# Kernel tuning notes

Hardware: AMD Instinct MI355X
Metric: run time of the kernel (lower is better)

The kernel has to match this reference:

```python
import jax, jax.numpy as jnp
import numpy as np

N, E, G, D, L = 20000, 320000, 256, 256, 5
EPS = 1e-5


def _bn(h, g, b):
    # BatchNorm1d in training mode: biased batch statistics over the row dim
    m = h.mean(axis=0)
    v = jnp.mean((h - m) ** 2, axis=0)
    return g * (h - m) / jnp.sqrt(v + EPS) + b


def setup_inputs() -> dict:
    key = jax.random.key(0)
    ks = iter(jax.random.split(key, 40))

    def rn(shape, s=0.1):
        return jax.random.normal(next(ks), shape, dtype=jnp.float32) * s

    inp = {}
    inp['x_feats'] = jax.random.randint(next(ks), (N, 6), 0, 4)
    inp['edge_index'] = jax.random.randint(next(ks), (2, E), 0, N)
    inp['edge_attr'] = jax.random.randint(next(ks), (E, 5), 0, 2)
    inp['batch'] = jnp.sort(jax.random.randint(next(ks), (N,), 0, G))
    inp['nt1'] = rn((119, D)); inp['nt2'] = rn((4, D)); inp['nt3'] = rn((7, D))
    inp['nt4'] = rn((8, D)); inp['nt5'] = rn((5, D)); inp['nt6'] = rn((7, D))
    inp['et1'] = rn((L, 5, D)); inp['et2'] = rn((L, 4, D)); inp['et3'] = rn((L, 2, D))
    inp['et4'] = rn((L, 2, D)); inp['et5'] = rn((L, 2, D))
    inp['w1'] = rn((L, 2 * D, D)); inp['b1'] = rn((L, 2 * D))
    inp['w2'] = rn((L, D, 2 * D)); inp['b2'] = rn((L, D))
    inp['bng'] = 1.0 + rn((L, D)); inp['bnb'] = rn((L, D))
    inp['pw'] = rn((3, D, D)); inp['pg'] = 1.0 + rn((3, D)); inp['pb'] = rn((3, D))
    inp['ow1'] = rn((D // 2, D)); inp['ob1'] = rn((D // 2,))
    inp['ow2'] = rn((2, D // 2)); inp['ob2'] = rn((2,))
    return inp


def reference(x_feats, edge_index, edge_attr, batch,
              nt1, nt2, nt3, nt4, nt5, nt6,
              et1, et2, et3, et4, et5,
              w1, b1, w2, b2, bng, bnb,
              pw, pg, pb, ow1, ob1, ow2, ob2):
    n = x_feats.shape[0]
    # atom embedding: sum of 6 feature embeddings -> [N, D]
    h = (nt1[x_feats[:, 0]] + nt2[x_feats[:, 1]] + nt3[x_feats[:, 2]]
         + nt4[x_feats[:, 3]] + nt5[x_feats[:, 4]] + nt6[x_feats[:, 5]])
    src, dst = edge_index[0], edge_index[1]
    for l in range(L):
        # edge embedding for real edges: [E, D]
        e = (et1[l][edge_attr[:, 0]] + et2[l][edge_attr[:, 1]] + et3[l][edge_attr[:, 2]]
             + et4[l][edge_attr[:, 3]] + et5[l][edge_attr[:, 4]])
        # self-loop edges carry attr [4,0,0,0,0]
        self_e = et1[l][4] + et2[l][0] + et3[l][0] + et4[l][0] + et5[l][0]
        # message = x_j + e, scatter-add into destinations; self loops add h + self_e
        aggr = jax.ops.segment_sum(h[src] + e, dst, num_segments=n) + h + self_e
        # GIN MLP update: D -> 2D -> D
        hh = jax.nn.relu(aggr @ w1[l].T + b1[l]) @ w2[l].T + b2[l]
        # batchnorm then relu (dropout=0; the layer==num_layer branch is unreachable)
        h = jax.nn.relu(_bn(hh, bng[l], bnb[l]))
    # global mean pool over graphs
    counts = jax.ops.segment_sum(jnp.ones((n, 1), h.dtype), batch, num_segments=G)
    hg = jax.ops.segment_sum(h, batch, num_segments=G) / jnp.maximum(counts, 1.0)
    # proj head: (Linear no-bias, BN, ReLU) x2, then Linear no-bias + BN
    for i in range(3):
        hg = _bn(hg @ pw[i].T, pg[i], pb[i])
        if i < 2:
            hg = jax.nn.relu(hg)
    # output MLP: Linear -> Softplus -> Linear
    return jax.nn.softplus(hg @ ow1.T + ob1) @ ow2.T + ob2
```

## Files before the change

### kernel.cpp

```cpp
#include <hip/hip_runtime.h>

#define DD 256
#define TWO_D 512
#define NLAYER 5
#define NGRAPH 256
#define BNEPS 1e-5f

typedef __attribute__((ext_vector_type(8))) _Float16 half8;
typedef __attribute__((ext_vector_type(4))) _Float16 half4;
typedef __attribute__((ext_vector_type(4))) float f32x4;
typedef __attribute__((address_space(1))) void gvoid_t;
typedef __attribute__((address_space(3))) void svoid_t;

__global__ __launch_bounds__(256) void embed_kernel(
    const int* __restrict__ xf,
    const float* __restrict__ nt1, const float* __restrict__ nt2,
    const float* __restrict__ nt3, const float* __restrict__ nt4,
    const float* __restrict__ nt5, const float* __restrict__ nt6,
    _Float16* __restrict__ h16, int* __restrict__ deg, int N)
{
  int i = blockIdx.x;
  int j = threadIdx.x;
  if (i >= N) return;
  if (j == 0) deg[i] = 0;
  int x0 = xf[i*6+0], x1 = xf[i*6+1], x2 = xf[i*6+2];
  int x3 = xf[i*6+3], x4 = xf[i*6+4], x5 = xf[i*6+5];
  float v = nt1[x0*DD+j] + nt2[x1*DD+j] + nt3[x2*DD+j]
          + nt4[x3*DD+j] + nt5[x4*DD+j] + nt6[x5*DD+j];
  h16[(size_t)i*DD + j] = (_Float16)v;
}

__global__ __launch_bounds__(256) void hist_pack_kernel(
    const int* __restrict__ ei, const int* __restrict__ ea,
    int* __restrict__ deg, int* __restrict__ packed, int E)
{
  int e = blockIdx.x*256 + threadIdx.x;
  if (e >= E) return;
  int src = ei[e];
  int dst = ei[E + e];
  int code = (ea[e*5+0]&1) | ((ea[e*5+1]&1)<<1) | ((ea[e*5+2]&1)<<2)
           | ((ea[e*5+3]&1)<<3) | ((ea[e*5+4]&1)<<4);
  packed[e] = src | (code << 16);
  atomicAdd(&deg[dst], 1);
}

__global__ __launch_bounds__(1024) void scan_kernel(
    const int* __restrict__ deg, int* __restrict__ row_start,
    int* __restrict__ cursor, int N)
{
  __shared__ int sh[1024];
  __shared__ int carry_s;
  int t = threadIdx.x;
  if (t == 0) carry_s = 0;
  __syncthreads();
  for (int base = 0; base < N; base += 1024) {
    int carry = carry_s;
    int idx = base + t;
    int v = (idx < N) ? deg[idx] : 0;
    sh[t] = v;
    __syncthreads();
    for (int off = 1; off < 1024; off <<= 1) {
      int x = (t >= off) ? sh[t - off] : 0;
      __syncthreads();
      sh[t] += x;
      __syncthreads();
    }
    int incl = sh[t];
    if (idx < N) { int ex = carry + incl - v; row_start[idx] = ex; cursor[idx] = ex; }
    __syncthreads();
    if (t == 1023) carry_s = carry + sh[1023];
    __syncthreads();
  }
  if (t == 0) row_start[N] = carry_s;
}

__global__ __launch_bounds__(256) void scatter_kernel(
    const int* __restrict__ ei, const int* __restrict__ packed,
    int* __restrict__ cursor, int* __restrict__ esort, int E)
{
  int e = blockIdx.x*256 + threadIdx.x;
  if (e >= E) return;
  int dst = ei[E + e];
  int pos = atomicAdd(&cursor[dst], 1);
  esort[pos] = packed[e];
}

__global__ __launch_bounds__(256) void wconv_kernel(
    const float* __restrict__ w1, const float* __restrict__ w2,
    _Float16* __restrict__ w1h, _Float16* __restrict__ w2h, int n)
{
  for (int i = blockIdx.x*256 + threadIdx.x; i < n; i += gridDim.x*256) {
    w1h[i] = (_Float16)w1[i];
    w2h[i] = (_Float16)w2[i];
  }
}

__global__ __launch_bounds__(256) void etab_kernel(
    const float* __restrict__ et1, const float* __restrict__ et2,
    const float* __restrict__ et3, const float* __restrict__ et4,
    const float* __restrict__ et5, _Float16* __restrict__ etab)
{
  int b = blockIdx.x;
  int l = b / 33, c = b % 33;
  int j = threadIdx.x;
  int a0 = (c==32)?4:(c&1);
  int a1 = (c==32)?0:((c>>1)&1);
  int a2 = (c==32)?0:((c>>2)&1);
  int a3 = (c==32)?0:((c>>3)&1);
  int a4 = (c==32)?0:((c>>4)&1);
  etab[((size_t)l*33 + c)*DD + j] = (_Float16)(
      et1[(l*5+a0)*DD+j] + et2[(l*4+a1)*DD+j] + et3[(l*2+a2)*DD+j]
    + et4[(l*2+a3)*DD+j] + et5[(l*2+a4)*DD+j]);
}

__global__ __launch_bounds__(256) void bn_prep_kernel(
    float* __restrict__ stats, const float* __restrict__ g, const float* __restrict__ b,
    float* __restrict__ scsh, float inv_n)
{
  int j = threadIdx.x;
  float m = stats[j] * inv_n;
  float var = fmaxf(stats[DD + j] * inv_n - m*m, 0.f);
  float sc = g[j] * rsqrtf(var + BNEPS);
  scsh[j] = sc;
  scsh[DD + j] = b[j] - m*sc;
  stats[j] = 0.f; stats[DD + j] = 0.f;
}

template<int APPLY_BN>
__global__ __launch_bounds__(256) void aggr_kernel(
    const _Float16* __restrict__ hsrc, const _Float16* __restrict__ etab_l,
    const int* __restrict__ row_start, const int* __restrict__ esort,
    const float* __restrict__ scsh,
    _Float16* __restrict__ aggrh, int N)
{
  __shared__ __attribute__((aligned(16))) _Float16 se[33*DD];
  for (int i = threadIdx.x; i < 33*DD/8; i += 256)
    ((int4*)se)[i] = ((const int4*)etab_l)[i];
  __syncthreads();
  const int wave = threadIdx.x >> 6, lane = threadIdx.x & 63;
  const int c4 = lane << 2;
  float sc0 = 1.f, sc1 = 1.f, sc2 = 1.f, sc3 = 1.f;
  float sh0 = 0.f, sh1 = 0.f, sh2 = 0.f, sh3 = 0.f;
  if (APPLY_BN) {
    sc0 = scsh[c4+0]; sc1 = scsh[c4+1]; sc2 = scsh[c4+2]; sc3 = scsh[c4+3];
    sh0 = scsh[DD+c4+0]; sh1 = scsh[DD+c4+1]; sh2 = scsh[DD+c4+2]; sh3 = scsh[DD+c4+3];
  }
  const int W0 = blockIdx.x*4 + wave, NW = gridDim.x*4;

#define BNX(h4, out0, out1, out2, out3)                                   \
  { float t0_ = (float)(h4).x, t1_ = (float)(h4).y,                       \
          t2_ = (float)(h4).z, t3_ = (float)(h4).w;                       \
    if (APPLY_BN) {                                                       \
      t0_ = fmaxf(t0_*sc0 + sh0, 0.f); t1_ = fmaxf(t1_*sc1 + sh1, 0.f);  \
      t2_ = fmaxf(t2_*sc2 + sh2, 0.f); t3_ = fmaxf(t3_*sc3 + sh3, 0.f);  \
    }                                                                     \
    out0 = t0_; out1 = t1_; out2 = t2_; out3 = t3_; }

  for (int node = W0; node < N; node += NW) {
    int p  = row_start[node];
    int pe = row_start[node+1];
    const half4 hv = *(const half4*)(hsrc + (size_t)node*DD + c4);
    const half4 sv = *(const half4*)(se + 32*DD + c4);
    float ax, ay, az, aw;
    BNX(hv, ax, ay, az, aw);
    ax += (float)sv.x; ay += (float)sv.y; az += (float)sv.z; aw += (float)sv.w;
    for (; p + 4 <= pe; p += 4) {
      int pk0 = esort[p], pk1 = esort[p+1], pk2 = esort[p+2], pk3 = esort[p+3];
      const half4 h0 = *(const half4*)(hsrc + (size_t)(pk0 & 0xffff)*DD + c4);
      const half4 h1 = *(const half4*)(hsrc + (size_t)(pk1 & 0xffff)*DD + c4);
      const half4 h2 = *(const half4*)(hsrc + (size_t)(pk2 & 0xffff)*DD + c4);
      const half4 h3 = *(const half4*)(hsrc + (size_t)(pk3 & 0xffff)*DD + c4);
      const half4 e0 = *(const half4*)(se + (pk0 >> 16)*DD + c4);
      const half4 e1 = *(const half4*)(se + (pk1 >> 16)*DD + c4);
      const half4 e2 = *(const half4*)(se + (pk2 >> 16)*DD + c4);
      const half4 e3 = *(const half4*)(se + (pk3 >> 16)*DD + c4);
      float b0x,b0y,b0z,b0w, b1x,b1y,b1z,b1w, b2x,b2y,b2z,b2w, b3x,b3y,b3z,b3w;
      BNX(h0, b0x,b0y,b0z,b0w); BNX(h1, b1x,b1y,b1z,b1w);
      BNX(h2, b2x,b2y,b2z,b2w); BNX(h3, b3x,b3y,b3z,b3w);
      ax += (b0x+(float)e0.x) + (b1x+(float)e1.x) + (b2x+(float)e2.x) + (b3x+(float)e3.x);
      ay += (b0y+(float)e0.y) + (b1y+(float)e1.y) + (b2y+(float)e2.y) + (b3y+(float)e3.y);
      az += (b0z+(float)e0.z) + (b1z+(float)e1.z) + (b2z+(float)e2.z) + (b3z+(float)e3.z);
      aw += (b0w+(float)e0.w) + (b1w+(float)e1.w) + (b2w+(float)e2.w) + (b3w+(float)e3.w);
    }
    for (; p < pe; ++p) {
      int pk = esort[p];
      const half4 hx = *(const half4*)(hsrc + (size_t)(pk & 0xffff)*DD + c4);
      const half4 ex = *(const half4*)(se + (pk >> 16)*DD + c4);
      float bx, by, bz, bw;
      BNX(hx, bx, by, bz, bw);
      ax += bx + (float)ex.x; ay += by + (float)ex.y;
      az += bz + (float)ex.z; aw += bw + (float)ex.w;
    }
    half4 o;
    o.x = (_Float16)ax; o.y = (_Float16)ay; o.z = (_Float16)az; o.w = (_Float16)aw;
    *(half4*)(aggrh + (size_t)node*DD + c4) = o;
  }
#undef BNX
}

template<int RELU, int STATS>
__global__ __launch_bounds__(256) void gemm_bt(
    const _Float16* __restrict__ A,
    const _Float16* __restrict__ B,
    const float* __restrict__ bias,
    _Float16* __restrict__ O,
    float* __restrict__ stats,
    int K, int Nw, int Nreal)
{
  __shared__ __attribute__((aligned(16))) _Float16 lA[128*32];
  __shared__ __attribute__((aligned(16))) _Float16 lB[128*32];
  const int NT = Nw >> 7;
  const int bm = blockIdx.x / NT, bn = blockIdx.x % NT;
  const int m0 = bm << 7, n0 = bn << 7;
  const int t = threadIdx.x;
  const int wave = t >> 6, lane = t & 63;
  const int wm = wave & 1, wn = wave >> 1;
  const int r15 = lane & 15, quad = lane >> 4;
  const int srow = lane >> 2, sq = (lane & 3) << 3;
  f32x4 acc[4][4] = {};
  for (int k0 = 0; k0 < K; k0 += 32) {
    __syncthreads();
#pragma unroll
    for (int i = 0; i < 2; ++i) {
      const int seg = wave*2 + i;
      const int row = seg*16 + srow;
      __builtin_amdgcn_global_load_lds((gvoid_t*)(A + (size_t)(m0+row)*K + k0 + sq),
                                       (svoid_t*)(lA + seg*512), 16, 0, 0);
      __builtin_amdgcn_global_load_lds((gvoid_t*)(B + (size_t)(n0+row)*K + k0 + sq),
                                       (svoid_t*)(lB + seg*512), 16, 0, 0);
    }
    __syncthreads();
    half8 af[4], bfr[4];
#pragma unroll
    for (int f = 0; f < 4; ++f) {
      af[f]  = *(const half8*)(lA + (((wm<<6) + (f<<4) + r15) << 5) + (quad<<3));
      bfr[f] = *(const half8*)(lB + (((wn<<6) + (f<<4) + r15) << 5) + (quad<<3));
    }
#pragma unroll
    for (int fm = 0; fm < 4; ++fm)
#pragma unroll
      for (int fn = 0; fn < 4; ++fn)
        acc[fm][fn] = __builtin_amdgcn_mfma_f32_16x16x32_f16(af[fm], bfr[fn], acc[fm][fn], 0, 0, 0);
  }
#pragma unroll
  for (int fn = 0; fn < 4; ++fn) {
    const int col = n0 + (wn<<6) + (fn<<4) + r15;
    const float bv = bias[col];
    float s1 = 0.f, s2 = 0.f;
#pragma unroll
    for (int fm = 0; fm < 4; ++fm) {
      const int rowb = m0 + (wm<<6) + (fm<<4) + (quad<<2);
#pragma unroll
      for (int r = 0; r < 4; ++r) {
        float v = acc[fm][fn][r] + bv;
        if (RELU) v = fmaxf(v, 0.f);
        O[(size_t)(rowb + r)*Nw + col] = (_Float16)v;
        if (STATS && (rowb + r < Nreal)) { s1 += v; s2 += v*v; }
      }
    }
    if (STATS) {
      s1 += __shfl_xor(s1, 16); s1 += __shfl_xor(s1, 32);
      s2 += __shfl_xor(s2, 16); s2 += __shfl_xor(s2, 32);
      if (lane < 16) { atomicAdd(&stats[col], s1); atomicAdd(&stats[DD + col], s2); }
    }
  }
}

__global__ __launch_bounds__(256) void zero_kernel(float* __restrict__ p, int n) {
  for (int i = blockIdx.x*256 + threadIdx.x; i < n; i += gridDim.x*256) p[i] = 0.f;
}

__global__ __launch_bounds__(256) void pool_kernel(
    const _Float16* __restrict__ hh16, const float* __restrict__ scsh,
    const int* __restrict__ batch,
    float* __restrict__ hgsum, int* __restrict__ hgcnt, int N)
{
  int j = threadIdx.x;
  float sc = scsh[j], sh = scsh[DD + j];
  int r0 = blockIdx.x * 64;
  int cur = -1; float acc = 0.f; int run = 0;
  for (int r = 0; r < 64; ++r) {
    int row = r0 + r;
    if (row >= N) break;
    int g = batch[row];
    if (g != cur) {
      if (cur >= 0) {
        atomicAdd(&hgsum[(size_t)cur*DD + j], acc);
        if (j == 0) atomicAdd(&hgcnt[cur], run);
      }
      cur = g; acc = 0.f; run = 0;
    }
    float v = (float)hh16[(size_t)row*DD + j];
    acc += fmaxf(v*sc + sh, 0.f);
    run++;
  }
  if (cur >= 0) {
    atomicAdd(&hgsum[(size_t)cur*DD + j], acc);
    if (j == 0) atomicAdd(&hgcnt[cur], run);
  }
}

__global__ __launch_bounds__(256) void hgfin_kernel(
    const float* __restrict__ hgsum, const int* __restrict__ hgcnt, float* __restrict__ hg)
{
  int g = blockIdx.x, j = threadIdx.x;
  float c = (float)max(hgcnt[g], 1);
  hg[(size_t)g*DD + j] = hgsum[(size_t)g*DD + j] / c;
}

__global__ __launch_bounds__(256) void proj_gemm_kernel(
    const float* __restrict__ in, const float* __restrict__ W,
    float* __restrict__ outb, float* __restrict__ pstat)
{
  __shared__ float sA[16][17];
  __shared__ float sB[16][17];
  int tx = threadIdx.x, ty = threadIdx.y;
  int r = blockIdx.y*16 + ty;
  int c = blockIdx.x*16 + tx;
  float acc = 0.f;
  for (int k0 = 0; k0 < DD; k0 += 16) {
    sA[ty][tx] = in[(size_t)r*DD + k0 + tx];
    sB[ty][tx] = W[(size_t)(blockIdx.x*16 + ty)*DD + k0 + tx];
    __syncthreads();
#pragma unroll
    for (int kk = 0; kk < 16; ++kk) acc += sA[ty][kk] * sB[tx][kk];
    __syncthreads();
  }
  outb[(size_t)r*DD + c] = acc;
  sA[ty][tx] = acc; sB[ty][tx] = acc*acc;
  __syncthreads();
  for (int o = 8; o > 0; o >>= 1) {
    if (ty < o) { sA[ty][tx] += sA[ty+o][tx]; sB[ty][tx] += sB[ty+o][tx]; }
    __syncthreads();
  }
  if (ty == 0) { atomicAdd(&pstat[c], sA[0][tx]); atomicAdd(&pstat[DD + c], sB[0][tx]); }
}

__global__ __launch_bounds__(256) void proj_bn_kernel(
    const float* __restrict__ tin, const float* __restrict__ pstat,
    const float* __restrict__ g, const float* __restrict__ b,
    float* __restrict__ outp, int do_relu)
{
  int c = threadIdx.x, r = blockIdx.x;
  float m = pstat[c] * (1.0f/NGRAPH);
  float var = fmaxf(pstat[DD + c] * (1.0f/NGRAPH) - m*m, 0.f);
  float sc = g[c] * rsqrtf(var + BNEPS);
  float sh = b[c] - m*sc;
  float v = tin[(size_t)r*DD + c]*sc + sh;
  outp[(size_t)r*DD + c] = do_relu ? fmaxf(v, 0.f) : v;
}

__global__ __launch_bounds__(128) void out_kernel(
    const float* __restrict__ hgf, const float* __restrict__ ow1,
    const float* __restrict__ ob1, const float* __restrict__ ow2,
    const float* __restrict__ ob2, float* __restrict__ outp)
{
  __shared__ float rowv[DD];
  __shared__ float z[128];
  int r = blockIdx.x, t = threadIdx.x;
  rowv[t] = hgf[(size_t)r*DD + t];
  rowv[t + 128] = hgf[(size_t)r*DD + t + 128];
  __syncthreads();
  float a = ob1[t];
  for (int k = 0; k < DD; ++k) a += rowv[k] * ow1[(size_t)t*DD + k];
  z[t] = fmaxf(a, 0.f) + log1pf(expf(-fabsf(a)));
  __syncthreads();
  if (t < 2) {
    float o = ob2[t];
    for (int k = 0; k < 128; ++k) o += z[k] * ow2[t*128 + k];
    outp[r*2 + t] = o;
  }
}

extern "C" void kernel_launch(void* const* d_in, const int* in_sizes, int n_in,
                              void* d_out, int out_size, void* d_ws, size_t ws_size,
                              hipStream_t stream)
{
  const int* x_feats = (const int*)d_in[0];
  const int* ei      = (const int*)d_in[1];
  const int* ea      = (const int*)d_in[2];
  const int* batch   = (const int*)d_in[3];
  const float* nt1 = (const float*)d_in[4];
  const float* nt2 = (const float*)d_in[5];
  const float* nt3 = (const float*)d_in[6];
  const float* nt4 = (const float*)d_in[7];
  const float* nt5 = (const float*)d_in[8];
  const float* nt6 = (const float*)d_in[9];
  const float* et1 = (const float*)d_in[10];
  const float* et2 = (const float*)d_in[11];
  const float* et3 = (const float*)d_in[12];
  const float* et4 = (const float*)d_in[13];
  const float* et5 = (const float*)d_in[14];
  const float* w1  = (const float*)d_in[15];
  const float* b1  = (const float*)d_in[16];
  const float* w2  = (const float*)d_in[17];
  const float* b2  = (const float*)d_in[18];
  const float* bng = (const float*)d_in[19];
  const float* bnb = (const float*)d_in[20];
  const float* pw  = (const float*)d_in[21];
  const float* pg  = (const float*)d_in[22];
  const float* pb  = (const float*)d_in[23];
  const float* ow1 = (const float*)d_in[24];
  const float* ob1 = (const float*)d_in[25];
  const float* ow2 = (const float*)d_in[26];
  const float* ob2 = (const float*)d_in[27];

  const int N = in_sizes[0] / 6;
  const int E = in_sizes[1] / 2;
  const int Mp = ((N + 127) >> 7) << 7;

  unsigned char* wp = (unsigned char*)d_ws;
  size_t off = 0;
  auto carve = [&](size_t bytes) -> void* {
    void* p = wp + off;
    off += (bytes + 255) & ~(size_t)255;
    return p;
  };

  _Float16* h16      = (_Float16*)carve((size_t)N * DD * 2);
  _Float16* aggrh    = (_Float16*)carve((size_t)Mp * DD * 2);
  _Float16* hh16     = (_Float16*)carve((size_t)Mp * DD * 2);
  _Float16* hidh     = (_Float16*)carve((size_t)Mp * TWO_D * 2);
  _Float16* w1h      = (_Float16*)carve((size_t)NLAYER * TWO_D * DD * 2);
  _Float16* w2h      = (_Float16*)carve((size_t)NLAYER * TWO_D * DD * 2);
  _Float16* etabg    = (_Float16*)carve((size_t)NLAYER * 33 * DD * 2);
  float* scsh        = (float*)carve(2 * DD * 4);
  int* deg           = (int*)carve((size_t)N * 4);
  int* row_start     = (int*)carve((size_t)(N + 1) * 4);
  int* cursor        = (int*)carve((size_t)N * 4);
  int* packed        = (int*)carve((size_t)E * 4);
  int* esort         = (int*)carve((size_t)E * 4);
  float* stats       = (float*)carve(2 * DD * 4);
  float* hgsum       = (float*)carve((size_t)NGRAPH * DD * 4);
  int* hgcnt         = (int*)carve((size_t)NGRAPH * 4);
  float* pstats      = (float*)carve(3 * 2 * DD * 4);
  float* hgA         = (float*)carve((size_t)NGRAPH * DD * 4);
  float* hgB         = (float*)carve((size_t)NGRAPH * DD * 4);
  float* t0          = (float*)carve((size_t)NGRAPH * DD * 4);
  (void)ws_size; (void)n_in; (void)out_size;

  const int EB = (E + 255) / 256;
  const float inv_n = 1.0f / (float)N;

  embed_kernel<<<N, 256, 0, stream>>>(x_feats, nt1, nt2, nt3, nt4, nt5, nt6, h16, deg, N);
  hist_pack_kernel<<<EB, 256, 0, stream>>>(ei, ea, deg, packed, E);
  scan_kernel<<<1, 1024, 0, stream>>>(deg, row_start, cursor, N);
  scatter_kernel<<<EB, 256, 0, stream>>>(ei, packed, cursor, esort, E);
  wconv_kernel<<<1024, 256, 0, stream>>>(w1, w2, w1h, w2h, NLAYER * TWO_D * DD);
  etab_kernel<<<NLAYER * 33, 256, 0, stream>>>(et1, et2, et3, et4, et5, etabg);
  zero_kernel<<<128, 256, 0, stream>>>(stats, 2*DD + NGRAPH*DD + NGRAPH + 3*2*DD);

  const int gm = Mp >> 7;
  for (int l = 0; l < NLAYER; ++l) {
    if (l == 0) {
      aggr_kernel<0><<<2048, 256, 0, stream>>>(h16, etabg, row_start, esort,
                                               nullptr, aggrh, N);
    } else {
      bn_prep_kernel<<<1, 256, 0, stream>>>(stats, bng + (l-1)*DD, bnb + (l-1)*DD,
                                            scsh, inv_n);
      aggr_kernel<1><<<2048, 256, 0, stream>>>(hh16, etabg + (size_t)l*33*DD,
                                               row_start, esort, scsh, aggrh, N);
    }
    gemm_bt<1,0><<<gm * (TWO_D >> 7), 256, 0, stream>>>(
        aggrh, w1h + (size_t)l*TWO_D*DD, b1 + l*TWO_D, hidh, nullptr,
        DD, TWO_D, N);
    gemm_bt<0,1><<<gm * (DD >> 7), 256, 0, stream>>>(
        hidh, w2h + (size_t)l*DD*TWO_D, b2 + l*DD, hh16, stats,
        TWO_D, DD, N);
  }
  bn_prep_kernel<<<1, 256, 0, stream>>>(stats, bng + (NLAYER-1)*DD, bnb + (NLAYER-1)*DD,
                                        scsh, inv_n);
  pool_kernel<<<(N + 63) / 64, 256, 0, stream>>>(hh16, scsh, batch, hgsum, hgcnt, N);
  hgfin_kernel<<<NGRAPH, 256, 0, stream>>>(hgsum, hgcnt, hgA);

  dim3 pgrid(16, 16), pblk(16, 16);
  proj_gemm_kernel<<<pgrid, pblk, 0, stream>>>(hgA, pw + 0*DD*DD, t0, pstats + 0*2*DD);
  proj_bn_kernel<<<NGRAPH, 256, 0, stream>>>(t0, pstats + 0*2*DD, pg + 0*DD, pb + 0*DD, hgB, 1);
  proj_gemm_kernel<<<pgrid, pblk, 0, stream>>>(hgB, pw + 1*DD*DD, t0, pstats + 1*2*DD);
  proj_bn_kernel<<<NGRAPH, 256, 0, stream>>>(t0, pstats + 1*2*DD, pg + 1*DD, pb + 1*DD, hgA, 1);
  proj_gemm_kernel<<<pgrid, pblk, 0, stream>>>(hgA, pw + 2*DD*DD, t0, pstats + 2*2*DD);
  proj_bn_kernel<<<NGRAPH, 256, 0, stream>>>(t0, pstats + 2*2*DD, pg + 2*DD, pb + 2*DD, hgB, 0);

  out_kernel<<<NGRAPH, 128, 0, stream>>>(hgB, ow1, ob1, ow2, ob2, (float*)d_out);
}
```

Before: 597.0 us.

## Merge setup kernels, fold BN prep into consumers, stage GEMM epilogue through LDS

Merges embedding, weight conversion, edge-table build, zeroing and edge packing into one prep kernel, and splits the degree histogram into its own kernel. BatchNorm scale/shift is now computed inside the aggregation, pooling, projection and output kernels, with per-layer stats buffers. This removes the bn_prep, hgfin and proj_bn launches. The scan now does a chunked serial scan per thread instead of looping over blocks, and the GEMM epilogue stages results in LDS so global stores are 16-byte coalesced, at the cost of extra syncs.

```diff
diff --git a/kernel.cpp b/kernel.cpp
--- a/kernel.cpp
+++ b/kernel.cpp
@@ -12,36 +12,79 @@
 typedef __attribute__((address_space(1))) void gvoid_t;
 typedef __attribute__((address_space(3))) void svoid_t;
 
-__global__ __launch_bounds__(256) void embed_kernel(
+__global__ __launch_bounds__(256) void prep_kernel(
     const int* __restrict__ xf,
     const float* __restrict__ nt1, const float* __restrict__ nt2,
     const float* __restrict__ nt3, const float* __restrict__ nt4,
     const float* __restrict__ nt5, const float* __restrict__ nt6,
-    _Float16* __restrict__ h16, int* __restrict__ deg, int N)
-{
-  int i = blockIdx.x;
-  int j = threadIdx.x;
-  if (i >= N) return;
-  if (j == 0) deg[i] = 0;
-  int x0 = xf[i*6+0], x1 = xf[i*6+1], x2 = xf[i*6+2];
-  int x3 = xf[i*6+3], x4 = xf[i*6+4], x5 = xf[i*6+5];
-  float v = nt1[x0*DD+j] + nt2[x1*DD+j] + nt3[x2*DD+j]
-          + nt4[x3*DD+j] + nt5[x4*DD+j] + nt6[x5*DD+j];
-  h16[(size_t)i*DD + j] = (_Float16)v;
-}
-
-__global__ __launch_bounds__(256) void hist_pack_kernel(
+    _Float16* __restrict__ h16,
+    const float* __restrict__ w1, const float* __restrict__ w2,
+    _Float16* __restrict__ w1h, _Float16* __restrict__ w2h,
+    const float* __restrict__ et1, const float* __restrict__ et2,
+    const float* __restrict__ et3, const float* __restrict__ et4,
+    const float* __restrict__ et5, _Float16* __restrict__ etab,
+    int* __restrict__ deg, int* __restrict__ zr, int zr_words,
     const int* __restrict__ ei, const int* __restrict__ ea,
-    int* __restrict__ deg, int* __restrict__ packed, int E)
+    int* __restrict__ packed,
+    int N, int E)
+{
+  const int t = threadIdx.x;
+  const int b = blockIdx.x;
+  const int B_EMB = N;
+  const int B_WC  = 128;
+  const int B_ET  = NLAYER * 33;
+  const int B_ZR  = 96;
+
+  if (b < B_EMB) {
+    int i = b, j = t;
+    int x0 = xf[i*6+0], x1 = xf[i*6+1], x2 = xf[i*6+2];
+    int x3 = xf[i*6+3], x4 = xf[i*6+4], x5 = xf[i*6+5];
+    float v = nt1[x0*DD+j] + nt2[x1*DD+j] + nt3[x2*DD+j]
+            + nt4[x3*DD+j] + nt5[x4*DD+j] + nt6[x5*DD+j];
+    h16[(size_t)i*DD + j] = (_Float16)v;
+  } else if (b < B_EMB + B_WC) {
+    int bid = b - B_EMB;
+    int n = NLAYER * TWO_D * DD;
+    for (int i = bid*256 + t; i < n; i += B_WC*256) {
+      w1h[i] = (_Float16)w1[i];
+      w2h[i] = (_Float16)w2[i];
+    }
+  } else if (b < B_EMB + B_WC + B_ET) {
+    int bid = b - B_EMB - B_WC;
+    int l = bid / 33, c = bid % 33;
+    int j = t;
+    int a0 = (c==32)?4:(c&1);
+    int a1 = (c==32)?0:((c>>1)&1);
+    int a2 = (c==32)?0:((c>>2)&1);
+    int a3 = (c==32)?0:((c>>3)&1);
+    int a4 = (c==32)?0:((c>>4)&1);
+    etab[((size_t)l*33 + c)*DD + j] = (_Float16)(
+        et1[(l*5+a0)*DD+j] + et2[(l*4+a1)*DD+j] + et3[(l*2+a2)*DD+j]
+      + et4[(l*2+a3)*DD+j] + et5[(l*2+a4)*DD+j]);
+  } else if (b < B_EMB + B_WC + B_ET + B_ZR) {
+    int bid = b - B_EMB - B_WC - B_ET;
+    int tw = N + zr_words;
+    for (int i = bid*256 + t; i < tw; i += B_ZR*256) {
+      if (i < N) deg[i] = 0;
+      else zr[i - N] = 0;
+    }
+  } else {
+    int bid = b - B_EMB - B_WC - B_ET - B_ZR;
+    int e = bid*256 + t;
+    if (e < E) {
+      int src = ei[e];
+      int code = (ea[e*5+0]&1) | ((ea[e*5+1]&1)<<1) | ((ea[e*5+2]&1)<<2)
+               | ((ea[e*5+3]&1)<<3) | ((ea[e*5+4]&1)<<4);
+      packed[e] = src | (code << 16);
+    }
+  }
+}
+
+__global__ __launch_bounds__(256) void hist_kernel(
+    const int* __restrict__ ei, int* __restrict__ deg, int E)
 {
   int e = blockIdx.x*256 + threadIdx.x;
-  if (e >= E) return;
-  int src = ei[e];
-  int dst = ei[E + e];
-  int code = (ea[e*5+0]&1) | ((ea[e*5+1]&1)<<1) | ((ea[e*5+2]&1)<<2)
-           | ((ea[e*5+3]&1)<<3) | ((ea[e*5+4]&1)<<4);
-  packed[e] = src | (code << 16);
-  atomicAdd(&deg[dst], 1);
+  if (e < E) atomicAdd(&deg[ei[E + e]], 1);
 }
 
 __global__ __launch_bounds__(1024) void scan_kernel(
@@ -49,29 +92,26 @@
     int* __restrict__ cursor, int N)
 {
   __shared__ int sh[1024];
-  __shared__ int carry_s;
   int t = threadIdx.x;
-  if (t == 0) carry_s = 0;
+  const int CH = (N + 1023) >> 10;
+  int base = t * CH;
+  int lim = N - base; if (lim < 0) lim = 0; if (lim > CH) lim = CH;
+  int s = 0;
+  for (int i = 0; i < lim; ++i) s += deg[base + i];
+  sh[t] = s;
   __syncthreads();
-  for (int base = 0; base < N; base += 1024) {
-    int carry = carry_s;
-    int idx = base + t;
-    int v = (idx < N) ? deg[idx] : 0;
-    sh[t] = v;
-    __syncthreads();
-    for (int off = 1; off < 1024; off <<= 1) {
-      int x = (t >= off) ? sh[t - off] : 0;
-      __syncthreads();
-      sh[t] += x;
-      __syncthreads();
-    }
-    int incl = sh[t];
-    if (idx < N) { int ex = carry + incl - v; row_start[idx] = ex; cursor[idx] = ex; }
-    __syncthreads();
-    if (t == 1023) carry_s = carry + sh[1023];
-    __syncthreads();
-  }
-  if (t == 0) row_start[N] = carry_s;
+  for (int off = 1; off < 1024; off <<= 1) {
+    int x = (t >= off) ? sh[t - off] : 0;
+    __syncthreads();
+    sh[t] += x;
+    __syncthreads();
+  }
+  int run = t ? sh[t-1] : 0;
+  for (int i = 0; i < lim; ++i) {
+    row_start[base+i] = run; cursor[base+i] = run;
+    run += deg[base+i];
+  }
+  if (t == 1023) row_start[N] = sh[1023];
 }
 
 __global__ __launch_bounds__(256) void scatter_kernel(
@@ -85,52 +125,12 @@
   esort[pos] = packed[e];
 }
 
-__global__ __launch_bounds__(256) void wconv_kernel(
-    const float* __restrict__ w1, const float* __restrict__ w2,
-    _Float16* __restrict__ w1h, _Float16* __restrict__ w2h, int n)
-{
-  for (int i = blockIdx.x*256 + threadIdx.x; i < n; i += gridDim.x*256) {
-    w1h[i] = (_Float16)w1[i];
-    w2h[i] = (_Float16)w2[i];
-  }
-}
-
-__global__ __launch_bounds__(256) void etab_kernel(
-    const float* __restrict__ et1, const float* __restrict__ et2,
-    const float* __restrict__ et3, const float* __restrict__ et4,
-    const float* __restrict__ et5, _Float16* __restrict__ etab)
-{
-  int b = blockIdx.x;
-  int l = b / 33, c = b % 33;
-  int j = threadIdx.x;
-  int a0 = (c==32)?4:(c&1);
-  int a1 = (c==32)?0:((c>>1)&1);
-  int a2 = (c==32)?0:((c>>2)&1);
-  int a3 = (c==32)?0:((c>>3)&1);
-  int a4 = (c==32)?0:((c>>4)&1);
-  etab[((size_t)l*33 + c)*DD + j] = (_Float16)(
-      et1[(l*5+a0)*DD+j] + et2[(l*4+a1)*DD+j] + et3[(l*2+a2)*DD+j]
-    + et4[(l*2+a3)*DD+j] + et5[(l*2+a4)*DD+j]);
-}
-
-__global__ __launch_bounds__(256) void bn_prep_kernel(
-    float* __restrict__ stats, const float* __restrict__ g, const float* __restrict__ b,
-    float* __restrict__ scsh, float inv_n)
-{
-  int j = threadIdx.x;
-  float m = stats[j] * inv_n;
-  float var = fmaxf(stats[DD + j] * inv_n - m*m, 0.f);
-  float sc = g[j] * rsqrtf(var + BNEPS);
-  scsh[j] = sc;
-  scsh[DD + j] = b[j] - m*sc;
-  stats[j] = 0.f; stats[DD + j] = 0.f;
-}
-
 template<int APPLY_BN>
 __global__ __launch_bounds__(256) void aggr_kernel(
     const _Float16* __restrict__ hsrc, const _Float16* __restrict__ etab_l,
     const int* __restrict__ row_start, const int* __restrict__ esort,
-    const float* __restrict__ scsh,
+    const float* __restrict__ stats_prev, const float* __restrict__ g,
+    const float* __restrict__ bb, float inv_n,
     _Float16* __restrict__ aggrh, int N)
 {
   __shared__ __attribute__((aligned(16))) _Float16 se[33*DD];
@@ -139,22 +139,24 @@
   __syncthreads();
   const int wave = threadIdx.x >> 6, lane = threadIdx.x & 63;
   const int c4 = lane << 2;
-  float sc0 = 1.f, sc1 = 1.f, sc2 = 1.f, sc3 = 1.f;
-  float sh0 = 0.f, sh1 = 0.f, sh2 = 0.f, sh3 = 0.f;
+  float sc0=1.f, sc1=1.f, sc2=1.f, sc3=1.f, sh0=0.f, sh1=0.f, sh2=0.f, sh3=0.f;
   if (APPLY_BN) {
-    sc0 = scsh[c4+0]; sc1 = scsh[c4+1]; sc2 = scsh[c4+2]; sc3 = scsh[c4+3];
-    sh0 = scsh[DD+c4+0]; sh1 = scsh[DD+c4+1]; sh2 = scsh[DD+c4+2]; sh3 = scsh[DD+c4+3];
+#define MKSC(k, SC, SH) { float m_ = stats_prev[c4+k]*inv_n;                      \
+    float v_ = fmaxf(stats_prev[DD+c4+k]*inv_n - m_*m_, 0.f);                     \
+    SC = g[c4+k]*rsqrtf(v_+BNEPS); SH = bb[c4+k] - m_*SC; }
+    MKSC(0, sc0, sh0) MKSC(1, sc1, sh1) MKSC(2, sc2, sh2) MKSC(3, sc3, sh3)
+#undef MKSC
   }
   const int W0 = blockIdx.x*4 + wave, NW = gridDim.x*4;
 
-#define BNX(h4, out0, out1, out2, out3)                                   \
+#define BNX(h4, o0, o1, o2, o3)                                           \
   { float t0_ = (float)(h4).x, t1_ = (float)(h4).y,                       \
           t2_ = (float)(h4).z, t3_ = (float)(h4).w;                       \
     if (APPLY_BN) {                                                       \
       t0_ = fmaxf(t0_*sc0 + sh0, 0.f); t1_ = fmaxf(t1_*sc1 + sh1, 0.f);  \
       t2_ = fmaxf(t2_*sc2 + sh2, 0.f); t3_ = fmaxf(t3_*sc3 + sh3, 0.f);  \
     }                                                                     \
-    out0 = t0_; out1 = t1_; out2 = t2_; out3 = t3_; }
+    o0 = t0_; o1 = t1_; o2 = t2_; o3 = t3_; }
 
   for (int node = W0; node < N; node += NW) {
     int p  = row_start[node];
@@ -207,8 +209,9 @@
     float* __restrict__ stats,
     int K, int Nw, int Nreal)
 {
-  __shared__ __attribute__((aligned(16))) _Float16 lA[128*32];
-  __shared__ __attribute__((aligned(16))) _Float16 lB[128*32];
+  __shared__ __attribute__((aligned(16))) _Float16 smem[8192];
+  _Float16* lA = smem;
+  _Float16* lB = smem + 4096;
   const int NT = Nw >> 7;
   const int bm = blockIdx.x / NT, bn = blockIdx.x % NT;
   const int m0 = bm << 7, n0 = bn << 7;
@@ -242,53 +245,68 @@
       for (int fn = 0; fn < 4; ++fn)
         acc[fm][fn] = __builtin_amdgcn_mfma_f32_16x16x32_f16(af[fm], bfr[fn], acc[fm][fn], 0, 0, 0);
   }
+  float bv[4];
+#pragma unroll
+  for (int fn = 0; fn < 4; ++fn) bv[fn] = bias[n0 + (wn<<6) + (fn<<4) + r15];
+  __syncthreads();
+  _Float16* tb = smem;
 #pragma unroll
   for (int fn = 0; fn < 4; ++fn) {
-    const int col = n0 + (wn<<6) + (fn<<4) + r15;
-    const float bv = bias[col];
     float s1 = 0.f, s2 = 0.f;
 #pragma unroll
     for (int fm = 0; fm < 4; ++fm) {
-      const int rowb = m0 + (wm<<6) + (fm<<4) + (quad<<2);
+      const int lr = (wm<<6) + (fm<<4) + (quad<<2);
 #pragma unroll
       for (int r = 0; r < 4; ++r) {
-        float v = acc[fm][fn][r] + bv;
+        float v = acc[fm][fn][r] + bv[fn];
         if (RELU) v = fmaxf(v, 0.f);
-        O[(size_t)(rowb + r)*Nw + col] = (_Float16)v;
-        if (STATS && (rowb + r < Nreal)) { s1 += v; s2 += v*v; }
+        tb[(lr + r)*40 + (wn<<4) + r15] = (_Float16)v;
+        if (STATS && (m0 + lr + r < Nreal)) { s1 += v; s2 += v*v; }
       }
     }
     if (STATS) {
       s1 += __shfl_xor(s1, 16); s1 += __shfl_xor(s1, 32);
       s2 += __shfl_xor(s2, 16); s2 += __shfl_xor(s2, 32);
-      if (lane < 16) { atomicAdd(&stats[col], s1); atomicAdd(&stats[DD + col], s2); }
-    }
-  }
-}
-
-__global__ __launch_bounds__(256) void zero_kernel(float* __restrict__ p, int n) {
-  for (int i = blockIdx.x*256 + threadIdx.x; i < n; i += gridDim.x*256) p[i] = 0.f;
+      if (lane < 16) {
+        const int col = n0 + (wn<<6) + (fn<<4) + r15;
+        atomicAdd(&stats[col], s1); atomicAdd(&stats[DD + col], s2);
+      }
+    }
+    __syncthreads();
+#pragma unroll
+    for (int it = 0; it < 2; ++it) {
+      int p = t + (it << 8);
+      int row = p & 127, strip = (p >> 7) & 1, hsel = p >> 8;
+      half8 vv = *(const half8*)(tb + row*40 + (strip<<4) + (hsel<<3));
+      *(half8*)(O + (size_t)(m0+row)*Nw + n0 + (strip<<6) + (fn<<4) + (hsel<<3)) = vv;
+    }
+    __syncthreads();
+  }
 }
 
 __global__ __launch_bounds__(256) void pool_kernel(
-    const _Float16* __restrict__ hh16, const float* __restrict__ scsh,
+    const _Float16* __restrict__ hh16, const float* __restrict__ stats_prev,
+    const float* __restrict__ g, const float* __restrict__ bb, float inv_n,
     const int* __restrict__ batch,
     float* __restrict__ hgsum, int* __restrict__ hgcnt, int N)
 {
   int j = threadIdx.x;
-  float sc = scsh[j], sh = scsh[DD + j];
+  float m = stats_prev[j]*inv_n;
+  float var = fmaxf(stats_prev[DD+j]*inv_n - m*m, 0.f);
+  float sc = g[j]*rsqrtf(var + BNEPS);
+  float sh = bb[j] - m*sc;
   int r0 = blockIdx.x * 64;
   int cur = -1; float acc = 0.f; int run = 0;
   for (int r = 0; r < 64; ++r) {
     int row = r0 + r;
     if (row >= N) break;
-    int g = batch[row];
-    if (g != cur) {
+    int gg = batch[row];
+    if (gg != cur) {
       if (cur >= 0) {
         atomicAdd(&hgsum[(size_t)cur*DD + j], acc);
         if (j == 0) atomicAdd(&hgcnt[cur], run);
       }
-      cur = g; acc = 0.f; run = 0;
+      cur = gg; acc = 0.f; run = 0;
     }
     float v = (float)hh16[(size_t)row*DD + j];
     acc += fmaxf(v*sc + sh, 0.f);
@@ -300,16 +318,12 @@
   }
 }
 
-__global__ __launch_bounds__(256) void hgfin_kernel(
-    const float* __restrict__ hgsum, const int* __restrict__ hgcnt, float* __restrict__ hg)
-{
-  int g = blockIdx.x, j = threadIdx.x;
-  float c = (float)max(hgcnt[g], 1);
-  hg[(size_t)g*DD + j] = hgsum[(size_t)g*DD + j] / c;
-}
-
+template<int MODE>
 __global__ __launch_bounds__(256) void proj_gemm_kernel(
-    const float* __restrict__ in, const float* __restrict__ W,
+    const float* __restrict__ in, const int* __restrict__ cnt,
+    const float* __restrict__ pstat_prev,
+    const float* __restrict__ gprev, const float* __restrict__ bprev,
+    const float* __restrict__ W,
     float* __restrict__ outb, float* __restrict__ pstat)
 {
   __shared__ float sA[16][17];
@@ -319,7 +333,17 @@
   int c = blockIdx.x*16 + tx;
   float acc = 0.f;
   for (int k0 = 0; k0 < DD; k0 += 16) {
-    sA[ty][tx] = in[(size_t)r*DD + k0 + tx];
+    int k = k0 + tx;
+    float a = in[(size_t)r*DD + k];
+    if (MODE == 0) {
+      a /= (float)max(cnt[r], 1);
+    } else {
+      float m = pstat_prev[k] * (1.0f/NGRAPH);
+      float var = fmaxf(pstat_prev[DD + k] * (1.0f/NGRAPH) - m*m, 0.f);
+      float sc = gprev[k] * rsqrtf(var + BNEPS);
+      a = fmaxf((a - m)*sc + bprev[k], 0.f);
+    }
+    sA[ty][tx] = a;
     sB[ty][tx] = W[(size_t)(blockIdx.x*16 + ty)*DD + k0 + tx];
     __syncthreads();
 #pragma unroll
@@ -336,30 +360,24 @@
   if (ty == 0) { atomicAdd(&pstat[c], sA[0][tx]); atomicAdd(&pstat[DD + c], sB[0][tx]); }
 }
 
-__global__ __launch_bounds__(256) void proj_bn_kernel(
-    const float* __restrict__ tin, const float* __restrict__ pstat,
-    const float* __restrict__ g, const float* __restrict__ b,
-    float* __restrict__ outp, int do_relu)
-{
-  int c = threadIdx.x, r = blockIdx.x;
-  float m = pstat[c] * (1.0f/NGRAPH);
-  float var = fmaxf(pstat[DD + c] * (1.0f/NGRAPH) - m*m, 0.f);
-  float sc = g[c] * rsqrtf(var + BNEPS);
-  float sh = b[c] - m*sc;
-  float v = tin[(size_t)r*DD + c]*sc + sh;
-  outp[(size_t)r*DD + c] = do_relu ? fmaxf(v, 0.f) : v;
-}
-
 __global__ __launch_bounds__(128) void out_kernel(
-    const float* __restrict__ hgf, const float* __restrict__ ow1,
-    const float* __restrict__ ob1, const float* __restrict__ ow2,
-    const float* __restrict__ ob2, float* __restrict__ outp)
+    const float* __restrict__ t2, const float* __restrict__ pstat2,
+    const float* __restrict__ g2, const float* __restrict__ b2p,
+    const float* __restrict__ ow1, const float* __restrict__ ob1,
+    const float* __restrict__ ow2, const float* __restrict__ ob2,
+    float* __restrict__ outp)
 {
   __shared__ float rowv[DD];
   __shared__ float z[128];
   int r = blockIdx.x, t = threadIdx.x;
-  rowv[t] = hgf[(size_t)r*DD + t];
-  rowv[t + 128] = hgf[(size_t)r*DD + t + 128];
+#pragma unroll
+  for (int half = 0; half < 2; ++half) {
+    int j = t + half*128;
+    float m = pstat2[j] * (1.0f/NGRAPH);
+    float var = fmaxf(pstat2[DD + j] * (1.0f/NGRAPH) - m*m, 0.f);
+    float sc = g2[j] * rsqrtf(var + BNEPS);
+    rowv[j] = (t2[(size_t)r*DD + j] - m)*sc + b2p[j];
+  }
   __syncthreads();
   float a = ob1[t];
   for (int k = 0; k < DD; ++k) a += rowv[k] * ow1[(size_t)t*DD + k];
@@ -424,62 +442,72 @@
   _Float16* w1h      = (_Float16*)carve((size_t)NLAYER * TWO_D * DD * 2);
   _Float16* w2h      = (_Float16*)carve((size_t)NLAYER * TWO_D * DD * 2);
   _Float16* etabg    = (_Float16*)carve((size_t)NLAYER * 33 * DD * 2);
-  float* scsh        = (float*)carve(2 * DD * 4);
   int* deg           = (int*)carve((size_t)N * 4);
   int* row_start     = (int*)carve((size_t)(N + 1) * 4);
   int* cursor        = (int*)carve((size_t)N * 4);
   int* packed        = (int*)carve((size_t)E * 4);
   int* esort         = (int*)carve((size_t)E * 4);
-  float* stats       = (float*)carve(2 * DD * 4);
+  float* stats       = (float*)carve((size_t)NLAYER * 2 * DD * 4);
   float* hgsum       = (float*)carve((size_t)NGRAPH * DD * 4);
   int* hgcnt         = (int*)carve((size_t)NGRAPH * 4);
   float* pstats      = (float*)carve(3 * 2 * DD * 4);
+  const int ZR_WORDS = NLAYER*2*DD + NGRAPH*DD + NGRAPH + 3*2*DD;
   float* hgA         = (float*)carve((size_t)NGRAPH * DD * 4);
   float* hgB         = (float*)carve((size_t)NGRAPH * DD * 4);
-  float* t0          = (float*)carve((size_t)NGRAPH * DD * 4);
+  float* t0c         = (float*)carve((size_t)NGRAPH * DD * 4);
   (void)ws_size; (void)n_in; (void)out_size;
 
   const int EB = (E + 255) / 256;
   const float inv_n = 1.0f / (float)N;
 
-  embed_kernel<<<N, 256, 0, stream>>>(x_feats, nt1, nt2, nt3, nt4, nt5, nt6, h16, deg, N);
-  hist_pack_kernel<<<EB, 256, 0, stream>>>(ei, ea, deg, packed, E);
+  const int PREP_BLOCKS = N + 128 + NLAYER*33 + 96 + EB;
+  prep_kernel<<<PREP_BLOCKS, 256, 0, stream>>>(
+      x_feats, nt1, nt2, nt3, nt4, nt5, nt6, h16,
+      w1, w2, w1h, w2h,
+      et1, et2, et3, et4, et5, etabg,
+      deg, (int*)stats, ZR_WORDS,
+      ei, ea, packed, N, E);
+  hist_kernel<<<EB, 256, 0, stream>>>(ei, deg, E);
   scan_kernel<<<1, 1024, 0, stream>>>(deg, row_start, cursor, N);
   scatter_kernel<<<EB, 256, 0, stream>>>(ei, packed, cursor, esort, E);
-  wconv_kernel<<<1024, 256, 0, stream>>>(w1, w2, w1h, w2h, NLAYER * TWO_D * DD);
-  etab_kernel<<<NLAYER * 33, 256, 0, stream>>>(et1, et2, et3, et4, et5, etabg);
-  zero_kernel<<<128, 256, 0, stream>>>(stats, 2*DD + NGRAPH*DD + NGRAPH + 3*2*DD);
 
   const int gm = Mp >> 7;
   for (int l = 0; l < NLAYER; ++l) {
+    float* st_prev = stats + (size_t)(l-1)*2*DD;
+    float* st_cur  = stats + (size_t)l*2*DD;
     if (l == 0) {
       aggr_kernel<0><<<2048, 256, 0, stream>>>(h16, etabg, row_start, esort,
-                                               nullptr, aggrh, N);
+                                               nullptr, nullptr, nullptr, inv_n,
+                                               aggrh, N);
     } else {
-      bn_prep_kernel<<<1, 256, 0, stream>>>(stats, bng + (l-1)*DD, bnb + (l-1)*DD,
-                                            scsh, inv_n);
       aggr_kernel<1><<<2048, 256, 0, stream>>>(hh16, etabg + (size_t)l*33*DD,
-                                               row_start, esort, scsh, aggrh, N);
+                                               row_start, esort,
+                                               st_prev, bng + (l-1)*DD, bnb + (l-1)*DD,
+                                               inv_n, aggrh, N);
     }
     gemm_bt<1,0><<<gm * (TWO_D >> 7), 256, 0, stream>>>(
         aggrh, w1h + (size_t)l*TWO_D*DD, b1 + l*TWO_D, hidh, nullptr,
         DD, TWO_D, N);
     gemm_bt<0,1><<<gm * (DD >> 7), 256, 0, stream>>>(
-        hidh, w2h + (size_t)l*DD*TWO_D, b2 + l*DD, hh16, stats,
+        hidh, w2h + (size_t)l*DD*TWO_D, b2 + l*DD, hh16, st_cur,
         TWO_D, DD, N);
   }
-  bn_prep_kernel<<<1, 256, 0, stream>>>(stats, bng + (NLAYER-1)*DD, bnb + (NLAYER-1)*DD,
-                                        scsh, inv_n);
-  pool_kernel<<<(N + 63) / 64, 256, 0, stream>>>(hh16, scsh, batch, hgsum, hgcnt, N);
-  hgfin_kernel<<<NGRAPH, 256, 0, stream>>>(hgsum, hgcnt, hgA);
+
+  pool_kernel<<<(N + 63) / 64, 256, 0, stream>>>(
+      hh16, stats + (size_t)(NLAYER-1)*2*DD, bng + (NLAYER-1)*DD, bnb + (NLAYER-1)*DD,
+      inv_n, batch, hgsum, hgcnt, N);
 
   dim3 pgrid(16, 16), pblk(16, 16);
-  proj_gemm_kernel<<<pgrid, pblk, 0, stream>>>(hgA, pw + 0*DD*DD, t0, pstats + 0*2*DD);
-  proj_bn_kernel<<<NGRAPH, 256, 0, stream>>>(t0, pstats + 0*2*DD, pg + 0*DD, pb + 0*DD, hgB, 1);
-  proj_gemm_kernel<<<pgrid, pblk, 0, stream>>>(hgB, pw + 1*DD*DD, t0, pstats + 1*2*DD);
-  proj_bn_kernel<<<NGRAPH, 256, 0, stream>>>(t0, pstats + 1*2*DD, pg + 1*DD, pb + 1*DD, hgA, 1);
-  proj_gemm_kernel<<<pgrid, pblk, 0, stream>>>(hgA, pw + 2*DD*DD, t0, pstats + 2*2*DD);
-  proj_bn_kernel<<<NGRAPH, 256, 0, stream>>>(t0, pstats + 2*2*DD, pg + 2*DD, pb + 2*DD, hgB, 0);
-
-  out_kernel<<<NGRAPH, 128, 0, stream>>>(hgB, ow1, ob1, ow2, ob2, (float*)d_out);
-}
+  proj_gemm_kernel<0><<<pgrid, pblk, 0, stream>>>(
+      hgsum, hgcnt, nullptr, nullptr, nullptr,
+      pw + 0*DD*DD, hgA, pstats + 0*2*DD);
+  proj_gemm_kernel<1><<<pgrid, pblk, 0, stream>>>(
+      hgA, nullptr, pstats + 0*2*DD, pg + 0*DD, pb + 0*DD,
+      pw + 1*DD*DD, hgB, pstats + 1*2*DD);
+  proj_gemm_kernel<1><<<pgrid, pblk, 0, stream>>>(
+      hgB, nullptr, pstats + 1*2*DD, pg + 1*DD, pb + 1*DD,
+      pw + 2*DD*DD, t0c, pstats + 2*2*DD);
+  out_kernel<<<NGRAPH, 128, 0, stream>>>(
+      t0c, pstats + 2*2*DD, pg + 2*DD, pb + 2*DD,
+      ow1, ob1, ow2, ob2, (float*)d_out);
+}
```

New measurement: 586.2 us. About the same (-1.8%).
